# Performance work log

Hardware: AMD Instinct MI355X
Metric: run time of the kernel (lower is better)

## Reference

```python
import jax, jax.numpy as jnp
import numpy as np

N_HEADS = 16
EMBED = 1024
T = 2048        # given tokens
CACHE_NUM = 1024  # prepended cache tokens (x[0,-1] in the original)


def setup_inputs() -> dict:
    key = jax.random.key(0)
    k1, k2 = jax.random.split(key)
    qkv = jax.random.normal(k1, (T, 3 * EMBED), dtype=jnp.float32)
    # In the original these cache rows are torch.randn generated inside forward;
    # we lift them into a deterministic explicit input with identical semantics.
    cache = jax.random.normal(k2, (CACHE_NUM, 3 * EMBED), dtype=jnp.float32)
    return {"qkv": qkv, "cache": cache}


def reference(qkv, cache):
    C = EMBED
    H = N_HEADS
    D = C // H  # head_dim = 64
    t = qkv.shape[0]
    tc = cache.shape[0]
    t_full = t + tc  # T_ in the original

    gq, gk, gv = jnp.split(qkv, 3, axis=1)      # each [T, C]
    cq, ck, cv = jnp.split(cache, 3, axis=1)    # each [cache_num, C]

    q = jnp.concatenate([cq, gq], axis=0)  # [T_, C]
    k = jnp.concatenate([ck, gk], axis=0)
    v = jnp.concatenate([cv, gv], axis=0)

    # [T_, C] -> [H, T_, D]
    q = q.reshape(t_full, H, D).transpose(1, 0, 2)
    k = k.reshape(t_full, H, D).transpose(1, 0, 2)
    v = v.reshape(t_full, H, D).transpose(1, 0, 2)

    scale = 1.0 / np.sqrt(D).astype(np.float32)
    att = jnp.einsum('htd,hsd->hts', q, k) * scale  # [H, T_, T_]

    causal = jnp.tril(jnp.ones((t_full, t_full), dtype=bool))
    att = jnp.where(causal[None, :, :], att, jnp.float32(-jnp.inf))
    att = jax.nn.softmax(att, axis=-1)
    # attn_dropout is identity in eval / p=0

    y = jnp.einsum('hts,hsd->htd', att, v)          # [H, T_, D]
    y = y.transpose(1, 0, 2).reshape(t_full, C)     # [T_, C]
    return y[tc:, :]                                # drop cache rows -> [T, C]
```

## Files before the change

kernel.cpp:

```cpp
#include <hip/hip_runtime.h>
#include <cmath>


typedef _Float16 f16;
typedef __attribute__((ext_vector_type(8))) _Float16 f16x8;
typedef __attribute__((ext_vector_type(4))) _Float16 f16x4;
typedef __attribute__((ext_vector_type(2))) _Float16 f16x2;
typedef __attribute__((ext_vector_type(4))) float    f32x4;

constexpr int TC  = 1024;
constexpr int C3  = 3072;
constexpr int CE  = 1024;
constexpr int NH  = 16;
constexpr int TQ  = 2048;
constexpr int NKT = 48;

constexpr size_t KV_ELEMS = (size_t)NH * NKT * 4096;

constexpr int SPLITS[16] = {2,2,3,3,3,3,4,4,4,4,5,5,5,5,6,6};
constexpr int PRE[16]    = {0,2,4,7,10,13,16,20,24,28,32,37,42,47,52,58};
constexpr int NSLOT      = 64;

constexpr size_t OPART_E = (size_t)NSLOT * NH * 128 * 64;
constexpr size_t LPART_F = (size_t)NSLOT * NH * 128;

__device__ __forceinline__ void dma16(const void* g, void* l) {
    __builtin_amdgcn_global_load_lds(
        (const __attribute__((address_space(1))) void*)g,
        (__attribute__((address_space(3))) void*)l, 16, 0, 0);
}

__device__ __forceinline__ f16x2 pkrtz(float a, float b) {
    return __builtin_bit_cast(f16x2, __builtin_amdgcn_cvt_pkrtz(a, b));
}

__global__ __launch_bounds__(256)
void prepass_f16(const float* __restrict__ qkv, const float* __restrict__ cache,
                 f16* __restrict__ Kt, f16* __restrict__ Vt)
{
    const int b   = blockIdx.x;
    const int h   = b & 15;
    const int kt  = b >> 4;
    const int tid = threadIdx.x;
    const int bt  = kt * 64;
    const float* src = (bt < TC) ? (cache + (size_t)bt * C3)
                                 : (qkv + (size_t)(bt - TC) * C3);
    f16* ktile = Kt + (size_t)(h * NKT + kt) * 4096;
    f16* vtile = Vt + (size_t)(h * NKT + kt) * 4096;

    __shared__ f16 vtmp[64 * 66];

    {
        const int tok = tid >> 2;
        const int c4  = tid & 3;
        const float* p = src + (size_t)tok * C3 + h * 64 + CE + c4 * 16;
        f32x4 x0 = ((const f32x4*)p)[0], x1 = ((const f32x4*)p)[1];
        f32x4 x2 = ((const f32x4*)p)[2], x3 = ((const f32x4*)p)[3];
        const int ch0 = (2 * c4)     ^ (tok & 7);
        const int ch1 = (2 * c4 + 1) ^ (tok & 7);
        *(f16x8*)&ktile[tok * 64 + ch0 * 8] =
            (f16x8){(f16)x0.x,(f16)x0.y,(f16)x0.z,(f16)x0.w,
                    (f16)x1.x,(f16)x1.y,(f16)x1.z,(f16)x1.w};
        *(f16x8*)&ktile[tok * 64 + ch1 * 8] =
            (f16x8){(f16)x2.x,(f16)x2.y,(f16)x2.z,(f16)x2.w,
                    (f16)x3.x,(f16)x3.y,(f16)x3.z,(f16)x3.w};
    }
    {
        const int tok  = tid >> 2;
        const int dblk = (tid & 3) * 16;
        const float* p = src + (size_t)tok * C3 + h * 64 + 2 * CE + dblk;
        f32x4 x0 = ((const f32x4*)p)[0], x1 = ((const f32x4*)p)[1];
        f32x4 x2 = ((const f32x4*)p)[2], x3 = ((const f32x4*)p)[3];
        float v[16] = {x0.x,x0.y,x0.z,x0.w, x1.x,x1.y,x1.z,x1.w,
                       x2.x,x2.y,x2.z,x2.w, x3.x,x3.y,x3.z,x3.w};
        f16* dst = &vtmp[tok * 66 + dblk];
        #pragma unroll
        for (int i = 0; i < 8; ++i)
            *(f16x2*)&dst[2 * i] = (f16x2){(f16)v[2 * i], (f16)v[2 * i + 1]};
    }
    __syncthreads();
    {
        const int d  = tid >> 2;
        const int tb = (tid & 3) * 16;
        f16 col[16];
        #pragma unroll
        for (int i = 0; i < 16; ++i) col[i] = vtmp[(tb + i) * 66 + d];
        const int c0 = tb >> 3;
        *(f16x8*)&vtile[d * 64 + ((c0 ^ (d & 7)) * 8)] =
            (f16x8){col[0],col[1],col[2],col[3],col[4],col[5],col[6],col[7]};
        *(f16x8*)&vtile[d * 64 + (((c0 + 1) ^ (d & 7)) * 8)] =
            (f16x8){col[8],col[9],col[10],col[11],col[12],col[13],col[14],col[15]};
    }
}

__global__ __launch_bounds__(256, 4)
void attn_splitk(const float* __restrict__ qkv,
                 const f16* __restrict__ Kt,
                 const f16* __restrict__ Vt,
                 f16*  __restrict__ Opart,
                 float* __restrict__ lpart,
                 float* __restrict__ out,
                 int direct)
{
    const int bb = blockIdx.x;
    int h, qt, s, nsp;
    if (direct) {
        h = bb & 15;
        const int idx = bb >> 4;
        qt = (h < 8) ? idx : 15 - idx;
        s = 0; nsp = 1;
    } else {
        h = bb >> 6;
        const int g = ((bb & 63) + h * 4) & 63;
        qt = 0;
        #pragma unroll
        for (int i = 1; i < 16; ++i) qt += (g >= PRE[i]) ? 1 : 0;
        s = g - PRE[qt];
        nsp = SPLITS[qt];
    }
    const int nkt = 2 * qt + 18;
    const int t0  = nkt * s / nsp;
    const int t1  = nkt * (s + 1) / nsp;

    const int tid  = threadIdx.x;
    const int w    = tid >> 6;
    const int lane = tid & 63;
    const int l15  = lane & 15;
    const int quad = lane >> 4;

    __shared__ __align__(16) f16 sKV[2][8192];

    const float qs = 0.125f * 1.44269504088896f;
    f16x8 qfrag[2][2];
    #pragma unroll
    for (int u = 0; u < 2; ++u) {
        const float* qp = qkv + (size_t)(qt * 128 + w * 32 + u * 16 + l15) * C3
                              + h * 64 + quad * 8;
        #pragma unroll
        for (int c = 0; c < 2; ++c) {
            f32x4 a = *(const f32x4*)(qp + c * 32);
            f32x4 b = *(const f32x4*)(qp + c * 32 + 4);
            qfrag[u][c] = (f16x8){(f16)(a.x * qs), (f16)(a.y * qs),
                                  (f16)(a.z * qs), (f16)(a.w * qs),
                                  (f16)(b.x * qs), (f16)(b.y * qs),
                                  (f16)(b.z * qs), (f16)(b.w * qs)};
        }
    }

    f32x4 o_accT[2][4];
    #pragma unroll
    for (int u = 0; u < 2; ++u)
        #pragma unroll
        for (int d = 0; d < 4; ++d) o_accT[u][d] = (f32x4){0.f, 0.f, 0.f, 0.f};
    float l_i[2] = {0.f, 0.f};

    const int qbase_w = TC + qt * 128 + w * 32;
    const int soff = w * 2048 + lane * 16;
    const char* kg = (const char*)(Kt + (size_t)(h * NKT + t0) * 4096) + soff;
    const char* vg = (const char*)(Vt + (size_t)(h * NKT + t0) * 4096) + soff;

    const int ksw = (quad ^ (l15 & 7)) * 8;

    {
        char* kl = (char*)&sKV[0][0]    + soff;
        char* vl = (char*)&sKV[0][4096] + soff;
        dma16(kg, kl);           dma16(kg + 1024, kl + 1024);
        dma16(vg, vl);           dma16(vg + 1024, vl + 1024);
    }
    int cur = 0;

    for (int kt = t0; kt < t1; ++kt) {
        __syncthreads();

        kg += 8192; vg += 8192;
        if (kt + 1 < t1) {
            char* kl = (char*)&sKV[cur ^ 1][0]    + soff;
            char* vl = (char*)&sKV[cur ^ 1][4096] + soff;
            dma16(kg, kl);       dma16(kg + 1024, kl + 1024);
            dma16(vg, vl);       dma16(vg + 1024, vl + 1024);
        }
        const f16* sK  = &sKV[cur][0];
        const f16* sVT = &sKV[cur][4096];
        cur ^= 1;

        f32x4 sacc[2][4];
        #pragma unroll
        for (int u = 0; u < 2; ++u)
            #pragma unroll
            for (int kb = 0; kb < 4; ++kb) sacc[u][kb] = (f32x4){0.f,0.f,0.f,0.f};
        #pragma unroll
        for (int kb = 0; kb < 4; ++kb) {
            const int ib = (kb * 16 + l15) * 64 + ksw;
            f16x8 a0 = *(const f16x8*)&sK[ib];
            f16x8 a1 = *(const f16x8*)&sK[ib ^ 32];
            #pragma unroll
            for (int u = 0; u < 2; ++u) {
                sacc[u][kb] = __builtin_amdgcn_mfma_f32_16x16x32_f16(a0, qfrag[u][0], sacc[u][kb], 0, 0, 0);
                sacc[u][kb] = __builtin_amdgcn_mfma_f32_16x16x32_f16(a1, qfrag[u][1], sacc[u][kb], 0, 0, 0);
            }
        }

        if (kt * 64 + 63 > qbase_w) {
            #pragma unroll
            for (int u = 0; u < 2; ++u) {
                const int qg = qbase_w + u * 16 + l15;
                #pragma unroll
                for (int kb = 0; kb < 4; ++kb) {
                    const int kq = kt * 64 + kb * 16 + quad * 4;
                    #pragma unroll
                    for (int r = 0; r < 4; ++r)
                        if (kq + r > qg) sacc[u][kb][r] = -INFINITY;
                }
            }
        }

        f16x4 pfrag[2][4];
        #pragma unroll
        for (int u = 0; u < 2; ++u) {
            float ls = 0.f;
            #pragma unroll
            for (int kb = 0; kb < 4; ++kb) {
                const float p0 = exp2f(sacc[u][kb][0]);
                const float p1 = exp2f(sacc[u][kb][1]);
                const float p2 = exp2f(sacc[u][kb][2]);
                const float p3 = exp2f(sacc[u][kb][3]);
                ls += (p0 + p1) + (p2 + p3);
                f16x2 lo = pkrtz(p0, p1);
                f16x2 hi = pkrtz(p2, p3);
                pfrag[u][kb] = __builtin_shufflevector(lo, hi, 0, 1, 2, 3);
            }
            l_i[u] += ls;
        }

        #pragma unroll
        for (int dblk = 0; dblk < 4; ++dblk) {
            const int row = dblk * 16 + l15;
            #pragma unroll
            for (int kb = 0; kb < 4; ++kb) {
                const int ch = (kb * 2 + (quad >> 1)) ^ (row & 7);
                f16x4 vf = *(const f16x4*)
                    &sVT[row * 64 + ch * 8 + (quad & 1) * 4];
                #pragma unroll
                for (int u = 0; u < 2; ++u)
                    o_accT[u][dblk] = __builtin_amdgcn_mfma_f32_16x16x16f16(
                        vf, pfrag[u][kb], o_accT[u][dblk], 0, 0, 0);
            }
        }
    }

    #pragma unroll
    for (int u = 0; u < 2; ++u) {
        float lf = l_i[u];
        lf += __shfl_xor(lf, 16);
        lf += __shfl_xor(lf, 32);
        const int qloc = w * 32 + u * 16 + l15;
        if (direct) {
            const float inv = 1.0f / lf;
            const int gq = qt * 128 + qloc;
            #pragma unroll
            for (int dblk = 0; dblk < 4; ++dblk) {
                f32x4 o = o_accT[u][dblk];
                o.x *= inv; o.y *= inv; o.z *= inv; o.w *= inv;
                *(f32x4*)&out[(size_t)gq * CE + h * 64 + dblk * 16 + quad * 4] = o;
            }
        } else {
            const int slot = PRE[qt] + s;
            f16*   op = Opart + ((size_t)slot * NH + h) * (128 * 64);
            float* lp = lpart + ((size_t)slot * NH + h) * 128;
            #pragma unroll
            for (int dblk = 0; dblk < 4; ++dblk) {
                f32x4 o = o_accT[u][dblk];
                f16x2 lo = pkrtz(o.x, o.y);
                f16x2 hi = pkrtz(o.z, o.w);
                *(f16x4*)&op[qloc * 64 + dblk * 16 + quad * 4] =
                    __builtin_shufflevector(lo, hi, 0, 1, 2, 3);
            }
            if (quad == 0) lp[qloc] = lf;
        }
    }
}

__global__ __launch_bounds__(256)
void combine_splits(const f16* __restrict__ Opart,
                    const float* __restrict__ lpart,
                    float* __restrict__ out)
{
    const int t  = blockIdx.x * 256 + threadIdx.x;
    const int d4 = t & 15;
    const int q  = (t >> 4) & (TQ - 1);
    const int h  = t >> 15;

    const int qt    = q >> 7;
    const int qloc  = q & 127;
    const int nsp   = SPLITS[qt];
    const int slot0 = PRE[qt];

    float lsum = 0.f;
    f32x4 acc = (f32x4){0.f, 0.f, 0.f, 0.f};
    for (int s = 0; s < nsp; ++s) {
        const size_t sb = (size_t)(slot0 + s) * NH + h;
        lsum += lpart[sb * 128 + qloc];
        f16x4 o = *(const f16x4*)&Opart[sb * (128 * 64) + qloc * 64 + d4 * 4];
        acc.x += (float)o[0]; acc.y += (float)o[1];
        acc.z += (float)o[2]; acc.w += (float)o[3];
    }
    const float inv = 1.0f / lsum;
    *(f32x4*)&out[(size_t)q * CE + h * 64 + d4 * 4] =
        (f32x4){acc.x * inv, acc.y * inv, acc.z * inv, acc.w * inv};
}

extern "C" void kernel_launch(void* const* d_in, const int* in_sizes, int n_in,
                              void* d_out, int out_size, void* d_ws, size_t ws_size,
                              hipStream_t stream)
{
    const float* qkv   = (const float*)d_in[0];
    const float* cache = (const float*)d_in[1];
    float*       out   = (float*)d_out;
    (void)in_sizes; (void)n_in; (void)out_size;

    const size_t kv_bytes = 2 * KV_ELEMS * sizeof(f16);
    const size_t need     = kv_bytes + OPART_E * sizeof(f16)
                          + LPART_F * sizeof(float);

    f16*   Kt    = (f16*)d_ws;
    f16*   Vt    = Kt + KV_ELEMS;
    f16*   Opart = (f16*)((char*)d_ws + kv_bytes);
    float* lpart = (float*)((char*)Opart + OPART_E * sizeof(f16));

    const int direct = (ws_size >= need) ? 0 : 1;

    prepass_f16<<<dim3(NH * NKT), dim3(256), 0, stream>>>(qkv, cache, Kt, Vt);
    attn_splitk<<<dim3(direct ? 256 : 1024), dim3(256), 0, stream>>>(
        qkv, Kt, Vt, Opart, lpart, out, direct);
    if (!direct) {
        combine_splits<<<dim3(NH * TQ * 16 / 256), dim3(256), 0, stream>>>(
            Opart, lpart, out);
    }
}
```

Measured before the change: 122.1 us.

## Single-buffer KV tile, double split count, raise occupancy, templatize direct path

Doubles the number of split-K partitions per query tile (128 slots instead of 64), so the attention kernel launches twice as many blocks. The double-buffered shared K/V tile becomes a single buffer, which halves LDS per block and allows the launch bound to rise to 6 blocks per CU. Prefetch of the next tile now waits until compute on the current tile finishes, behind an extra barrier, so load latency is hidden only by other resident blocks rather than by in-block overlap. The direct/split choice becomes a template parameter, and the combine kernel must now read more partial slots.

```diff
diff --git a/kernel.cpp b/kernel.cpp
--- a/kernel.cpp
+++ b/kernel.cpp
@@ -17,9 +17,9 @@
 
 constexpr size_t KV_ELEMS = (size_t)NH * NKT * 4096;
 
-constexpr int SPLITS[16] = {2,2,3,3,3,3,4,4,4,4,5,5,5,5,6,6};
-constexpr int PRE[16]    = {0,2,4,7,10,13,16,20,24,28,32,37,42,47,52,58};
-constexpr int NSLOT      = 64;
+constexpr int SPL2[16] = {4,5,5,6,6,7,7,8,8,9,9,10,10,11,11,12};
+constexpr int PRE2[16] = {0,4,9,14,20,26,33,40,48,56,65,74,84,94,105,116};
+constexpr int NSLOT    = 128;
 
 constexpr size_t OPART_E = (size_t)NSLOT * NH * 128 * 64;
 constexpr size_t LPART_F = (size_t)NSLOT * NH * 128;
@@ -93,34 +93,34 @@
     }
 }
 
-__global__ __launch_bounds__(256, 4)
-void attn_splitk(const float* __restrict__ qkv,
+template <bool DIRECT>
+__global__ __launch_bounds__(256, 6)
+void attn_kernel(const float* __restrict__ qkv,
                  const f16* __restrict__ Kt,
                  const f16* __restrict__ Vt,
                  f16*  __restrict__ Opart,
                  float* __restrict__ lpart,
-                 float* __restrict__ out,
-                 int direct)
+                 float* __restrict__ out)
 {
     const int bb = blockIdx.x;
     int h, qt, s, nsp;
-    if (direct) {
+    if (DIRECT) {
         h = bb & 15;
         const int idx = bb >> 4;
         qt = (h < 8) ? idx : 15 - idx;
         s = 0; nsp = 1;
     } else {
-        h = bb >> 6;
-        const int g = ((bb & 63) + h * 4) & 63;
+        h = bb >> 7;
+        const int g = ((bb & 127) + h * 8) & 127;
         qt = 0;
         #pragma unroll
-        for (int i = 1; i < 16; ++i) qt += (g >= PRE[i]) ? 1 : 0;
-        s = g - PRE[qt];
-        nsp = SPLITS[qt];
+        for (int i = 1; i < 16; ++i) qt += (g >= PRE2[i]) ? 1 : 0;
+        s = g - PRE2[qt];
+        nsp = SPL2[qt];
     }
     const int nkt = 2 * qt + 18;
-    const int t0  = nkt * s / nsp;
-    const int t1  = nkt * (s + 1) / nsp;
+    const int t0  = DIRECT ? 0 : (nkt * s / nsp);
+    const int t1  = DIRECT ? nkt : (nkt * (s + 1) / nsp);
 
     const int tid  = threadIdx.x;
     const int w    = tid >> 6;
@@ -128,7 +128,7 @@
     const int l15  = lane & 15;
     const int quad = lane >> 4;
 
-    __shared__ __align__(16) f16 sKV[2][8192];
+    __shared__ __align__(16) f16 sKV[8192];
 
     const float qs = 0.125f * 1.44269504088896f;
     f16x8 qfrag[2][2];
@@ -158,30 +158,19 @@
     const int soff = w * 2048 + lane * 16;
     const char* kg = (const char*)(Kt + (size_t)(h * NKT + t0) * 4096) + soff;
     const char* vg = (const char*)(Vt + (size_t)(h * NKT + t0) * 4096) + soff;
+    char* kl = (char*)sKV + soff;
+    char* vl = (char*)sKV + 8192 + soff;
 
     const int ksw = (quad ^ (l15 & 7)) * 8;
 
-    {
-        char* kl = (char*)&sKV[0][0]    + soff;
-        char* vl = (char*)&sKV[0][4096] + soff;
-        dma16(kg, kl);           dma16(kg + 1024, kl + 1024);
-        dma16(vg, vl);           dma16(vg + 1024, vl + 1024);
-    }
-    int cur = 0;
+    dma16(kg, kl);  dma16(kg + 1024, kl + 1024);
+    dma16(vg, vl);  dma16(vg + 1024, vl + 1024);
 
     for (int kt = t0; kt < t1; ++kt) {
         __syncthreads();
 
-        kg += 8192; vg += 8192;
-        if (kt + 1 < t1) {
-            char* kl = (char*)&sKV[cur ^ 1][0]    + soff;
-            char* vl = (char*)&sKV[cur ^ 1][4096] + soff;
-            dma16(kg, kl);       dma16(kg + 1024, kl + 1024);
-            dma16(vg, vl);       dma16(vg + 1024, vl + 1024);
-        }
-        const f16* sK  = &sKV[cur][0];
-        const f16* sVT = &sKV[cur][4096];
-        cur ^= 1;
+        const f16* sK  = &sKV[0];
+        const f16* sVT = &sKV[4096];
 
         f32x4 sacc[2][4];
         #pragma unroll
@@ -246,6 +235,13 @@
                         vf, pfrag[u][kb], o_accT[u][dblk], 0, 0, 0);
             }
         }
+
+        __syncthreads();
+        if (kt + 1 < t1) {
+            const size_t d = (size_t)(kt + 1 - t0) * 8192;
+            dma16(kg + d, kl);  dma16(kg + d + 1024, kl + 1024);
+            dma16(vg + d, vl);  dma16(vg + d + 1024, vl + 1024);
+        }
     }
 
     #pragma unroll
@@ -254,7 +250,7 @@
         lf += __shfl_xor(lf, 16);
         lf += __shfl_xor(lf, 32);
         const int qloc = w * 32 + u * 16 + l15;
-        if (direct) {
+        if (DIRECT) {
             const float inv = 1.0f / lf;
             const int gq = qt * 128 + qloc;
             #pragma unroll
@@ -264,7 +260,7 @@
                 *(f32x4*)&out[(size_t)gq * CE + h * 64 + dblk * 16 + quad * 4] = o;
             }
         } else {
-            const int slot = PRE[qt] + s;
+            const int slot = PRE2[qt] + s;
             f16*   op = Opart + ((size_t)slot * NH + h) * (128 * 64);
             float* lp = lpart + ((size_t)slot * NH + h) * 128;
             #pragma unroll
@@ -292,8 +288,8 @@
 
     const int qt    = q >> 7;
     const int qloc  = q & 127;
-    const int nsp   = SPLITS[qt];
-    const int slot0 = PRE[qt];
+    const int nsp   = SPL2[qt];
+    const int slot0 = PRE2[qt];
 
     float lsum = 0.f;
     f32x4 acc = (f32x4){0.f, 0.f, 0.f, 0.f};
@@ -327,13 +323,14 @@
     f16*   Opart = (f16*)((char*)d_ws + kv_bytes);
     float* lpart = (float*)((char*)Opart + OPART_E * sizeof(f16));
 
-    const int direct = (ws_size >= need) ? 0 : 1;
-
     prepass_f16<<<dim3(NH * NKT), dim3(256), 0, stream>>>(qkv, cache, Kt, Vt);
-    attn_splitk<<<dim3(direct ? 256 : 1024), dim3(256), 0, stream>>>(
-        qkv, Kt, Vt, Opart, lpart, out, direct);
-    if (!direct) {
+    if (ws_size >= need) {
+        attn_kernel<false><<<dim3(16 * NSLOT), dim3(256), 0, stream>>>(
+            qkv, Kt, Vt, Opart, lpart, out);
         combine_splits<<<dim3(NH * TQ * 16 / 256), dim3(256), 0, stream>>>(
             Opart, lpart, out);
-    }
-}
+    } else {
+        attn_kernel<true><<<dim3(256), dim3(256), 0, stream>>>(
+            qkv, Kt, Vt, Opart, lpart, out);
+    }
+}
```

New measurement: 267.2 us. 119% more time.

## Fuse split-K combine into attention kernel via last-block atomic counter

Applied to the files above, without the earlier changes.

Removes the separate combine_splits launch. Each split block now bumps a per-(head, q-tile) atomic counter, and the last block to finish sums the partial outputs and writes the normalized result. The counters are zeroed in the prepass kernel. The first K/V tile DMA is also hoisted ahead of the Q fragment load so the two overlap. This saves a kernel launch and a full pass over the partials, at the cost of a serialized reduction tail in the last block of each tile.

```diff
diff --git a/kernel.cpp b/kernel.cpp
--- a/kernel.cpp
+++ b/kernel.cpp
@@ -36,12 +36,16 @@
 
 __global__ __launch_bounds__(256)
 void prepass_f16(const float* __restrict__ qkv, const float* __restrict__ cache,
-                 f16* __restrict__ Kt, f16* __restrict__ Vt)
+                 f16* __restrict__ Kt, f16* __restrict__ Vt,
+                 int* __restrict__ cnt)
 {
     const int b   = blockIdx.x;
     const int h   = b & 15;
     const int kt  = b >> 4;
     const int tid = threadIdx.x;
+
+    if (b == 0) cnt[tid] = 0;
+
     const int bt  = kt * 64;
     const float* src = (bt < TC) ? (cache + (size_t)bt * C3)
                                  : (qkv + (size_t)(bt - TC) * C3);
@@ -99,6 +103,7 @@
                  const f16* __restrict__ Vt,
                  f16*  __restrict__ Opart,
                  float* __restrict__ lpart,
+                 int*   __restrict__ cnt,
                  float* __restrict__ out,
                  int direct)
 {
@@ -130,6 +135,18 @@
 
     __shared__ __align__(16) f16 sKV[2][8192];
 
+    const int qbase_w = TC + qt * 128 + w * 32;
+    const int soff = w * 2048 + lane * 16;
+    const char* kg = (const char*)(Kt + (size_t)(h * NKT + t0) * 4096) + soff;
+    const char* vg = (const char*)(Vt + (size_t)(h * NKT + t0) * 4096) + soff;
+
+    {
+        char* kl = (char*)&sKV[0][0]    + soff;
+        char* vl = (char*)&sKV[0][4096] + soff;
+        dma16(kg, kl);           dma16(kg + 1024, kl + 1024);
+        dma16(vg, vl);           dma16(vg + 1024, vl + 1024);
+    }
+
     const float qs = 0.125f * 1.44269504088896f;
     f16x8 qfrag[2][2];
     #pragma unroll
@@ -154,19 +171,7 @@
         for (int d = 0; d < 4; ++d) o_accT[u][d] = (f32x4){0.f, 0.f, 0.f, 0.f};
     float l_i[2] = {0.f, 0.f};
 
-    const int qbase_w = TC + qt * 128 + w * 32;
-    const int soff = w * 2048 + lane * 16;
-    const char* kg = (const char*)(Kt + (size_t)(h * NKT + t0) * 4096) + soff;
-    const char* vg = (const char*)(Vt + (size_t)(h * NKT + t0) * 4096) + soff;
-
     const int ksw = (quad ^ (l15 & 7)) * 8;
-
-    {
-        char* kl = (char*)&sKV[0][0]    + soff;
-        char* vl = (char*)&sKV[0][4096] + soff;
-        dma16(kg, kl);           dma16(kg + 1024, kl + 1024);
-        dma16(vg, vl);           dma16(vg + 1024, vl + 1024);
-    }
     int cur = 0;
 
     for (int kt = t0; kt < t1; ++kt) {
@@ -278,35 +283,43 @@
             if (quad == 0) lp[qloc] = lf;
         }
     }
-}
-
-__global__ __launch_bounds__(256)
-void combine_splits(const f16* __restrict__ Opart,
-                    const float* __restrict__ lpart,
-                    float* __restrict__ out)
-{
-    const int t  = blockIdx.x * 256 + threadIdx.x;
-    const int d4 = t & 15;
-    const int q  = (t >> 4) & (TQ - 1);
-    const int h  = t >> 15;
-
-    const int qt    = q >> 7;
-    const int qloc  = q & 127;
-    const int nsp   = SPLITS[qt];
-    const int slot0 = PRE[qt];
-
-    float lsum = 0.f;
-    f32x4 acc = (f32x4){0.f, 0.f, 0.f, 0.f};
-    for (int s = 0; s < nsp; ++s) {
-        const size_t sb = (size_t)(slot0 + s) * NH + h;
-        lsum += lpart[sb * 128 + qloc];
-        f16x4 o = *(const f16x4*)&Opart[sb * (128 * 64) + qloc * 64 + d4 * 4];
-        acc.x += (float)o[0]; acc.y += (float)o[1];
-        acc.z += (float)o[2]; acc.w += (float)o[3];
-    }
-    const float inv = 1.0f / lsum;
-    *(f32x4*)&out[(size_t)q * CE + h * 64 + d4 * 4] =
-        (f32x4){acc.x * inv, acc.y * inv, acc.z * inv, acc.w * inv};
+
+    if (!direct) {
+        __shared__ int lastflag;
+        __threadfence();
+        __syncthreads();
+        if (tid == 0)
+            lastflag = (atomicAdd(&cnt[h * 16 + qt], 1) == nsp - 1);
+        __syncthreads();
+        if (lastflag) {
+            __threadfence();
+            const int qloc = tid >> 1;
+            const int dh   = (tid & 1) * 32;
+            float acc[32];
+            #pragma unroll
+            for (int i = 0; i < 32; ++i) acc[i] = 0.f;
+            float lsum = 0.f;
+            for (int sp = 0; sp < nsp; ++sp) {
+                const size_t sb = (size_t)(PRE[qt] + sp) * NH + h;
+                lsum += lpart[sb * 128 + qloc];
+                const f16* p = &Opart[sb * (128 * 64) + qloc * 64 + dh];
+                #pragma unroll
+                for (int i = 0; i < 4; ++i) {
+                    f16x8 v = *(const f16x8*)(p + i * 8);
+                    #pragma unroll
+                    for (int j = 0; j < 8; ++j) acc[i * 8 + j] += (float)v[j];
+                }
+            }
+            const float inv = 1.0f / lsum;
+            float* po = &out[(size_t)(qt * 128 + qloc) * CE + h * 64 + dh];
+            #pragma unroll
+            for (int i = 0; i < 8; ++i) {
+                f32x4 o = (f32x4){acc[4*i] * inv, acc[4*i+1] * inv,
+                                  acc[4*i+2] * inv, acc[4*i+3] * inv};
+                *(f32x4*)(po + 4 * i) = o;
+            }
+        }
+    }
 }
 
 extern "C" void kernel_launch(void* const* d_in, const int* in_sizes, int n_in,
@@ -320,20 +333,17 @@
 
     const size_t kv_bytes = 2 * KV_ELEMS * sizeof(f16);
     const size_t need     = kv_bytes + OPART_E * sizeof(f16)
-                          + LPART_F * sizeof(float);
+                          + LPART_F * sizeof(float) + 256 * sizeof(int);
 
     f16*   Kt    = (f16*)d_ws;
     f16*   Vt    = Kt + KV_ELEMS;
     f16*   Opart = (f16*)((char*)d_ws + kv_bytes);
     float* lpart = (float*)((char*)Opart + OPART_E * sizeof(f16));
+    int*   cnt   = (int*)(lpart + LPART_F);
 
     const int direct = (ws_size >= need) ? 0 : 1;
 
-    prepass_f16<<<dim3(NH * NKT), dim3(256), 0, stream>>>(qkv, cache, Kt, Vt);
+    prepass_f16<<<dim3(NH * NKT), dim3(256), 0, stream>>>(qkv, cache, Kt, Vt, cnt);
     attn_splitk<<<dim3(direct ? 256 : 1024), dim3(256), 0, stream>>>(
-        qkv, Kt, Vt, Opart, lpart, out, direct);
-    if (!direct) {
-        combine_splits<<<dim3(NH * TQ * 16 / 256), dim3(256), 0, stream>>>(
-            Opart, lpart, out);
-    }
-}
+        qkv, Kt, Vt, Opart, lpart, cnt, out, direct);
+}
```

After: 358.7 us. 2.94x slower.
